# Optimization experiments

Measured on AMD Instinct MI355X. Metric: run time of the kernel, lower is better.

The kernel has to match this reference:

```python
import jax, jax.numpy as jnp
import numpy as np

N_NODES = 50000
N_EDGES = 800000
NUM_FEATURES = 128
DIM = 32
HEADS = 16
NUM_CLASSES = 2
NUM_GRAPHS = 64


def setup_inputs() -> dict:
    key = jax.random.key(0)
    ks = jax.random.split(key, 16)
    inv = lambda fan_in: 1.0 / np.sqrt(fan_in)
    inp = {
        "x": jax.random.normal(ks[0], (N_NODES, NUM_FEATURES), dtype=jnp.float32),
        "edge_index": jax.random.randint(ks[1], (2, N_EDGES), 0, N_NODES, dtype=jnp.int64),
        "batch": jnp.sort(jax.random.randint(ks[2], (N_NODES,), 0, NUM_GRAPHS, dtype=jnp.int64)),
        # conv1: GraphConv(num_features -> dim)
        "W1_rel": jax.random.uniform(ks[3], (NUM_FEATURES, DIM), jnp.float32, -inv(NUM_FEATURES), inv(NUM_FEATURES)),
        "b1_rel": jnp.zeros((DIM,), jnp.float32),
        "W1_root": jax.random.uniform(ks[4], (NUM_FEATURES, DIM), jnp.float32, -inv(NUM_FEATURES), inv(NUM_FEATURES)),
        # conv3: GATConv(dim -> dim, heads=16, concat)
        "Wg": jax.random.uniform(ks[5], (DIM, HEADS * DIM), jnp.float32, -inv(DIM), inv(DIM)),
        "att_src": jax.random.uniform(ks[6], (HEADS, DIM), jnp.float32, -inv(DIM), inv(DIM)),
        "att_dst": jax.random.uniform(ks[7], (HEADS, DIM), jnp.float32, -inv(DIM), inv(DIM)),
        "bg": jnp.zeros((HEADS * DIM,), jnp.float32),
        # conv5: GraphConv(dim*16 -> dim)
        "W5_rel": jax.random.uniform(ks[8], (HEADS * DIM, DIM), jnp.float32, -inv(HEADS * DIM), inv(HEADS * DIM)),
        "b5_rel": jnp.zeros((DIM,), jnp.float32),
        "W5_root": jax.random.uniform(ks[9], (HEADS * DIM, DIM), jnp.float32, -inv(HEADS * DIM), inv(HEADS * DIM)),
        # fc1, fc2
        "Wfc1": jax.random.uniform(ks[10], (DIM, DIM), jnp.float32, -inv(DIM), inv(DIM)),
        "bfc1": jnp.zeros((DIM,), jnp.float32),
        "Wfc2": jax.random.uniform(ks[11], (DIM, NUM_CLASSES), jnp.float32, -inv(DIM), inv(DIM)),
        "bfc2": jnp.zeros((NUM_CLASSES,), jnp.float32),
    }
    return inp


def _graph_conv(x, src, dst, W_rel, b_rel, W_root):
    # PyG GraphConv (aggr='add'): out = lin_rel(sum_{j->i} x_j) + lin_root(x_i)
    agg = jax.ops.segment_sum(x[src], dst, num_segments=N_NODES)
    return agg @ W_rel + b_rel + x @ W_root


def _gat_conv(x, src, dst, W, att_src, att_dst, b):
    # PyG GATConv with add_self_loops=True, concat=True, negative_slope=0.2.
    # Dropout on attention is inactive in eval mode.
    loops = jnp.arange(N_NODES, dtype=src.dtype)
    src = jnp.concatenate([src, loops])
    dst = jnp.concatenate([dst, loops])
    h = (x @ W).reshape(N_NODES, HEADS, DIM)            # [N,H,C]
    a_src = jnp.einsum("nhc,hc->nh", h, att_src)        # [N,H]
    a_dst = jnp.einsum("nhc,hc->nh", h, att_dst)
    e = jax.nn.leaky_relu(a_src[src] + a_dst[dst], 0.2)  # [E,H]
    # segment softmax over incoming edges of each destination node
    e_max = jax.ops.segment_max(e, dst, num_segments=N_NODES)
    e_max = jnp.where(jnp.isfinite(e_max), e_max, 0.0)
    ex = jnp.exp(e - e_max[dst])
    denom = jax.ops.segment_sum(ex, dst, num_segments=N_NODES)
    alpha = ex / (denom[dst] + 1e-16)                   # [E,H]
    out = jax.ops.segment_sum(alpha[:, :, None] * h[src], dst, num_segments=N_NODES)
    return out.reshape(N_NODES, HEADS * DIM) + b


def reference(x, edge_index, batch, W1_rel, b1_rel, W1_root, Wg, att_src, att_dst, bg,
              W5_rel, b5_rel, W5_root, Wfc1, bfc1, Wfc2, bfc2):
    src, dst = edge_index[0], edge_index[1]
    h = jax.nn.relu(_graph_conv(x, src, dst, W1_rel, b1_rel, W1_root))
    h = jax.nn.relu(_gat_conv(h, src, dst, Wg, att_src, att_dst, bg))
    h = jax.nn.relu(_graph_conv(h, src, dst, W5_rel, b5_rel, W5_root))
    g = jax.ops.segment_sum(h, batch, num_segments=NUM_GRAPHS)  # global_add_pool
    g = jax.nn.relu(g @ Wfc1 + bfc1)
    logits = g @ Wfc2 + bfc2
    return jax.nn.sigmoid(logits)
```

## Files before the change

kernel.cpp:

```cpp
#include <hip/hip_runtime.h>

#define N_NODES 50000
#define N_EDGES 800000
#define NFEAT 128
#define DIM 32
#define HEADS 16
#define NGRAPH 64


__device__ inline bool edges_are_i64(const int* raw) {
    int acc = 0;
#pragma unroll
    for (int i = 1; i < 16; i += 2) acc |= raw[2 * N_EDGES - 16 + i];
    return acc == 0;
}

__global__ __launch_bounds__(256) void decode_edges(const int* __restrict__ raw,
                                                    int* __restrict__ esrc,
                                                    int* __restrict__ edst) {
    const bool is64 = edges_are_i64(raw);
    int e = blockIdx.x * 256 + threadIdx.x;
    if (e < N_EDGES) {
        if (is64) { esrc[e] = raw[2 * e]; edst[e] = raw[2 * (N_EDGES + e)]; }
        else      { esrc[e] = raw[e];     edst[e] = raw[N_EDGES + e]; }
    }
}

__global__ __launch_bounds__(256) void decode_batch(const int* __restrict__ raw,
                                                    int* __restrict__ out) {
    int acc = 0;
#pragma unroll
    for (int i = 1; i < 16; i += 2) acc |= raw[N_NODES - 16 + i];
    const bool is64 = (acc == 0);
    int b = blockIdx.x * 256 + threadIdx.x;
    if (b < N_NODES) {
        int v = is64 ? raw[2 * b] : raw[b];
        out[b] = v < 0 ? 0 : (v >= NGRAPH ? NGRAPH - 1 : v);
    }
}

__global__ __launch_bounds__(256) void init_kernel(int* __restrict__ deg, float* __restrict__ gpool) {
    int i = blockIdx.x * 256 + threadIdx.x;
    if (i < N_NODES) deg[i] = 1;
    if (i < NGRAPH * DIM) gpool[i] = 0.f;
}

__device__ inline int clampN(int v) {
    return v < 0 ? 0 : (v >= N_NODES ? N_NODES - 1 : v);
}

__global__ __launch_bounds__(256) void hist_kernel(const int* __restrict__ edst, int* __restrict__ deg) {
    int e = blockIdx.x * 256 + threadIdx.x;
    if (e < N_EDGES) atomicAdd(&deg[clampN(edst[e])], 1);
}

__global__ __launch_bounds__(1024) void scan_kernel(const int* __restrict__ deg,
                                                    int* __restrict__ off, int* __restrict__ cur) {
    __shared__ int part[1024];
    const int t = threadIdx.x;
    const int CH = (N_NODES + 1023) / 1024;
    int b0 = t * CH, b1 = b0 + CH;
    if (b0 > N_NODES) b0 = N_NODES;
    if (b1 > N_NODES) b1 = N_NODES;
    int s = 0;
    for (int i = b0; i < b1; ++i) s += deg[i];
    part[t] = s;
    __syncthreads();
    for (int ofs = 1; ofs < 1024; ofs <<= 1) {
        int v = part[t];
        int u = (t >= ofs) ? part[t - ofs] : 0;
        __syncthreads();
        part[t] = v + u;
        __syncthreads();
    }
    int run = (t > 0) ? part[t - 1] : 0;
    for (int i = b0; i < b1; ++i) { off[i] = run; cur[i] = run; run += deg[i]; }
    if (t == 1023) off[N_NODES] = part[1023];
}

__global__ __launch_bounds__(256) void place_kernel(const int* __restrict__ esrc,
                                                    const int* __restrict__ edst,
                                                    int* __restrict__ cur, int* __restrict__ nbr) {
    int idx = blockIdx.x * 256 + threadIdx.x;
    if (idx >= N_EDGES + N_NODES) return;
    int d, v;
    if (idx < N_EDGES) { d = clampN(edst[idx]); v = clampN(esrc[idx]); }
    else { d = idx - N_EDGES; v = d; }
    int p = atomicAdd(&cur[d], 1);
    nbr[p] = v;
}

__global__ __launch_bounds__(256) void node_linear2(const float* __restrict__ x,
                                                    const float* __restrict__ Wa,
                                                    const float* __restrict__ Wb,
                                                    const float* __restrict__ bias_b,
                                                    float* __restrict__ xrb, int n) {
    constexpr int KC = 128;
    constexpr int NB = 8;
    __shared__ float sWt[2][32][KC + 4];
    __shared__ float sX[NB][KC];
    const int t = threadIdx.x;
    const int o = t & 63;
    const int mat = o >> 5;
    const int c = o & 31;
    const int sub = t >> 6;
    const int base = blockIdx.x * NB;

    for (int i = t; i < 2 * KC * 32; i += 256) {
        int m = i >= KC * 32;
        int j = i - m * KC * 32;
        int kk = j >> 5, cc = j & 31;
        sWt[m][cc][kk] = (m ? Wb : Wa)[kk * 32 + cc];
    }
    for (int i = t; i < NB * KC; i += 256) {
        int r = i >> 7, kk = i & (KC - 1);
        int node = base + r;
        sX[r][kk] = (node < n) ? x[(size_t)node * KC + kk] : 0.f;
    }
    __syncthreads();
    float acc[2] = {0.f, 0.f};
#pragma unroll 4
    for (int kv = 0; kv < KC / 4; ++kv) {
        const float4 w = *(const float4*)&sWt[mat][c][kv * 4];
#pragma unroll
        for (int s = 0; s < 2; ++s) {
            const float4 xv = *(const float4*)&sX[sub + s * 4][kv * 4];
            acc[s] += w.x * xv.x + w.y * xv.y + w.z * xv.z + w.w * xv.w;
        }
    }
    const float bb = (mat == 1) ? bias_b[c] : 0.f;
#pragma unroll
    for (int s = 0; s < 2; ++s) {
        int node = base + sub + s * 4;
        if (node < n) xrb[(size_t)node * 64 + mat * 32 + c] = acc[s] + bb;
    }
}

__global__ __launch_bounds__(256) void graphconv_gather(const float* __restrict__ xrb,
                                                        const int* __restrict__ off,
                                                        const int* __restrict__ nbr,
                                                        float* __restrict__ out) {
    int d = blockIdx.x * 4 + (threadIdx.x >> 6);
    if (d >= N_NODES) return;
    const int l = threadIdx.x & 63;
    const int c = l & 31, half = l >> 5;
    const int j0 = off[d], j1 = off[d + 1];
    float acc = 0.f;
    for (int j = j0 + half; j < j1; j += 2) acc += xrb[(size_t)nbr[j] * 64 + c];
    acc += __shfl_xor(acc, 32);
    acc += xrb[(size_t)d * 64 + 32 + c] - xrb[(size_t)d * 64 + c];
    if (half == 0) out[(size_t)d * 32 + c] = acc > 0.f ? acc : 0.f;
}

__global__ __launch_bounds__(1024) void attc_kernel(const float* __restrict__ Wg,
                                                    const float* __restrict__ attS,
                                                    const float* __restrict__ attD,
                                                    float* __restrict__ attc) {
    const int t = threadIdx.x;
    const int sd = t >> 9, k = (t >> 4) & 31, hd = t & 15;
    const float* att = sd ? attD : attS;
    float acc = 0.f;
#pragma unroll
    for (int c = 0; c < 32; ++c) acc += Wg[k * 512 + hd * 32 + c] * att[hd * 32 + c];
    attc[t] = acc;
}

__global__ __launch_bounds__(256) void gat_att(const float* __restrict__ h1,
                                               const float* __restrict__ attc,
                                               float* __restrict__ asrc,
                                               float* __restrict__ adst) {
    __shared__ float sh1[8][32];
    __shared__ float sattc[1024];
    const int t = threadIdx.x;
    for (int i = t; i < 1024; i += 256) sattc[i] = attc[i];
    {
        int n0 = t >> 5, k = t & 31;
        sh1[n0][k] = h1[(size_t)(blockIdx.x * 8 + n0) * 32 + k];
    }
    __syncthreads();
    const int nl = t >> 5, hd = (t >> 1) & 15, sd = t & 1;
    float acc = 0.f;
#pragma unroll
    for (int k = 0; k < 32; ++k) acc += sh1[nl][k] * sattc[sd * 512 + k * 16 + hd];
    (sd ? adst : asrc)[(size_t)(blockIdx.x * 8 + nl) * 16 + hd] = acc;
}

__global__ __launch_bounds__(512) void gat_mega(const float* __restrict__ h1,
                                                const float* __restrict__ asrc,
                                                const float* __restrict__ adst,
                                                const int* __restrict__ off,
                                                const int* __restrict__ nbr,
                                                const float* __restrict__ Wg,
                                                const float* __restrict__ bg,
                                                const float* __restrict__ W5_rel,
                                                const float* __restrict__ W5_root,
                                                const float* __restrict__ b5,
                                                float* __restrict__ xrb) {
    __shared__ float sh_agg[8][512];
    __shared__ float sh_h2[8][512];
    __shared__ float spart[8][8][64];
    const int t = threadIdx.x;
    const int w = t >> 6, l = t & 63;
    const int d = blockIdx.x * 8 + w;

    {
        const int hd = l & 15;
        const int kb = (l >> 4) << 3;
        const float adst_v = adst[(size_t)d * 16 + hd];
        const int j0 = off[d], j1 = off[d + 1];
        float m = -1e30f;
        for (int j = j0; j < j1; ++j) {
            int s = nbr[j];
            float e = asrc[(size_t)s * 16 + hd] + adst_v;
            e = e < 0.f ? 0.2f * e : e;
            m = fmaxf(m, e);
        }
        float den = 0.f;
        float4 acca = {0.f, 0.f, 0.f, 0.f}, accb = {0.f, 0.f, 0.f, 0.f};
        for (int j = j0; j < j1; ++j) {
            int s = nbr[j];
            float e = asrc[(size_t)s * 16 + hd] + adst_v;
            e = e < 0.f ? 0.2f * e : e;
            float ex = expf(e - m);
            den += ex;
            const float4 ha = *(const float4*)&h1[(size_t)s * 32 + kb];
            const float4 hb = *(const float4*)&h1[(size_t)s * 32 + kb + 4];
            acca.x += ex * ha.x; acca.y += ex * ha.y; acca.z += ex * ha.z; acca.w += ex * ha.w;
            accb.x += ex * hb.x; accb.y += ex * hb.y; accb.z += ex * hb.z; accb.w += ex * hb.w;
        }
        const float r = 1.f / (den + 1e-16f);
        acca.x *= r; acca.y *= r; acca.z *= r; acca.w *= r;
        accb.x *= r; accb.y *= r; accb.z *= r; accb.w *= r;
        *(float4*)&sh_agg[w][hd * 32 + kb] = acca;
        *(float4*)&sh_agg[w][hd * 32 + kb + 4] = accb;
    }
    __syncthreads();

    {
        const int hh = (t >> 5) << 5;
        float acc[8] = {0.f, 0.f, 0.f, 0.f, 0.f, 0.f, 0.f, 0.f};
        for (int k = 0; k < 32; ++k) {
            const float wv = Wg[k * 512 + t];
#pragma unroll
            for (int nl = 0; nl < 8; ++nl) acc[nl] += sh_agg[nl][hh + k] * wv;
        }
        const float bgv = bg[t];
#pragma unroll
        for (int nl = 0; nl < 8; ++nl) {
            float v = acc[nl] + bgv;
            sh_h2[nl][t] = v > 0.f ? v : 0.f;
        }
    }
    __syncthreads();

    {
        const float* wp = (l < 32) ? (W5_rel + l) : (W5_root + (l - 32));
        float acc[8] = {0.f, 0.f, 0.f, 0.f, 0.f, 0.f, 0.f, 0.f};
        const int c0 = w * 64;
        for (int cc = 0; cc < 64; ++cc) {
            const int col = c0 + cc;
            const float wv = wp[(size_t)col * 32];
#pragma unroll
            for (int nl = 0; nl < 8; ++nl) acc[nl] += sh_h2[nl][col] * wv;
        }
#pragma unroll
        for (int nl = 0; nl < 8; ++nl) spart[w][nl][l] = acc[nl];
    }
    __syncthreads();

    {
        float acc = (l >= 32) ? b5[l - 32] : 0.f;
#pragma unroll
        for (int ww = 0; ww < 8; ++ww) acc += spart[ww][w][l];
        xrb[(size_t)(blockIdx.x * 8 + w) * 64 + l] = acc;
    }
}

__global__ __launch_bounds__(256) void pool_kernel(const float* __restrict__ h3,
                                                   const int* __restrict__ batch,
                                                   float* __restrict__ g) {
    const int KRUN = 32;
    int c = threadIdx.x & 31;
    int grp = blockIdx.x * 8 + (threadIdx.x >> 5);
    int n0 = grp * KRUN;
    if (n0 >= N_NODES) return;
    int nend = n0 + KRUN;
    if (nend > N_NODES) nend = N_NODES;
    float acc = 0.f;
    int curb = -1;
    for (int nn = n0; nn < nend; ++nn) {
        int b = batch[nn];
        if (b != curb) {
            if (curb >= 0) atomicAdd(&g[curb * 32 + c], acc);
            acc = 0.f;
            curb = b;
        }
        acc += h3[(size_t)nn * 32 + c];
    }
    if (curb >= 0) atomicAdd(&g[curb * 32 + c], acc);
}

__global__ __launch_bounds__(256) void final_head(const float* __restrict__ g,
                                                  const float* __restrict__ Wfc1,
                                                  const float* __restrict__ bfc1,
                                                  const float* __restrict__ Wfc2,
                                                  const float* __restrict__ bfc2,
                                                  float* __restrict__ out) {
    __shared__ float sg[NGRAPH * 32];
    __shared__ float s1[NGRAPH * 32];
    const int t = threadIdx.x;
    for (int i = t; i < NGRAPH * 32; i += 256) sg[i] = g[i];
    __syncthreads();
    for (int i = t; i < NGRAPH * 32; i += 256) {
        int gi = i >> 5, c = i & 31;
        float acc = bfc1[c];
#pragma unroll
        for (int k = 0; k < 32; ++k) acc += sg[gi * 32 + k] * Wfc1[k * 32 + c];
        s1[i] = acc > 0.f ? acc : 0.f;
    }
    __syncthreads();
    if (t < NGRAPH * 2) {
        int gi = t >> 1, cls = t & 1;
        float acc = bfc2[cls];
#pragma unroll
        for (int k = 0; k < 32; ++k) acc += s1[gi * 32 + k] * Wfc2[k * 2 + cls];
        out[t] = 1.f / (1.f + expf(-acc));
    }
}

extern "C" void kernel_launch(void* const* d_in, const int* in_sizes, int n_in,
                              void* d_out, int out_size, void* d_ws, size_t ws_size,
                              hipStream_t stream) {
    const float* x       = (const float*)d_in[0];
    const int*   eraw    = (const int*)d_in[1];
    const int*   braw    = (const int*)d_in[2];
    const float* W1_rel  = (const float*)d_in[3];
    const float* b1_rel  = (const float*)d_in[4];
    const float* W1_root = (const float*)d_in[5];
    const float* Wg      = (const float*)d_in[6];
    const float* attS    = (const float*)d_in[7];
    const float* attD    = (const float*)d_in[8];
    const float* bg      = (const float*)d_in[9];
    const float* W5_rel  = (const float*)d_in[10];
    const float* b5_rel  = (const float*)d_in[11];
    const float* W5_root = (const float*)d_in[12];
    const float* Wfc1    = (const float*)d_in[13];
    const float* bfc1    = (const float*)d_in[14];
    const float* Wfc2    = (const float*)d_in[15];
    const float* bfc2    = (const float*)d_in[16];
    float* out = (float*)d_out;

    float* f     = (float*)d_ws;
    float* xrb   = f;
    float* h1    = xrb + (size_t)N_NODES * 64;
    float* asrc  = h1 + (size_t)N_NODES * 32;
    float* adst  = asrc + (size_t)N_NODES * 16;
    float* attc  = adst + (size_t)N_NODES * 16;
    float* gpool = attc + 1024;
    int* esrcd   = (int*)(gpool + 2048);
    int* edstd   = esrcd + N_EDGES;
    int* batchd  = edstd + N_EDGES;
    int* deg     = batchd + N_NODES;
    int* off     = deg + (N_NODES + 1);
    int* cur     = off + (N_NODES + 1);
    int* nbr     = cur + N_NODES;

    decode_edges<<<(N_EDGES + 255) / 256, 256, 0, stream>>>(eraw, esrcd, edstd);
    decode_batch<<<(N_NODES + 255) / 256, 256, 0, stream>>>(braw, batchd);
    init_kernel<<<(N_NODES + 255) / 256, 256, 0, stream>>>(deg, gpool);
    hist_kernel<<<(N_EDGES + 255) / 256, 256, 0, stream>>>(edstd, deg);
    scan_kernel<<<1, 1024, 0, stream>>>(deg, off, cur);
    place_kernel<<<(N_EDGES + N_NODES + 255) / 256, 256, 0, stream>>>(esrcd, edstd, cur, nbr);

    node_linear2<<<(N_NODES + 7) / 8, 256, 0, stream>>>(x, W1_rel, W1_root, b1_rel, xrb, N_NODES);
    graphconv_gather<<<(N_NODES + 3) / 4, 256, 0, stream>>>(xrb, off, nbr, h1);

    attc_kernel<<<1, 1024, 0, stream>>>(Wg, attS, attD, attc);
    gat_att<<<(N_NODES + 7) / 8, 256, 0, stream>>>(h1, attc, asrc, adst);
    gat_mega<<<N_NODES / 8, 512, 0, stream>>>(h1, asrc, adst, off, nbr, Wg, bg,
                                              W5_rel, W5_root, b5_rel, xrb);

    graphconv_gather<<<(N_NODES + 3) / 4, 256, 0, stream>>>(xrb, off, nbr, h1);

    pool_kernel<<<((N_NODES + 31) / 32 + 7) / 8, 256, 0, stream>>>(h1, batchd, gpool);
    final_head<<<1, 256, 0, stream>>>(gpool, Wfc1, bfc1, Wfc2, bfc2, out);
}
```

Before: 820.5 us.

## Split GAT megakernel into gather and FFN kernels, fuse histogram into decode

Splits the fused GAT kernel into a smaller-block attention gather that writes the per-node aggregate to a global buffer and a separate FFN kernel that applies Wg and the W5 projections. This is meant to raise occupancy for the latency-bound gather at the cost of an extra 100MB-scale round trip through memory. The split only runs when the workspace is large enough; otherwise the old megakernel, now with unrolled loops and reused shared memory, is used. The change also fuses the degree histogram into edge decoding, removes redundant clamps, and unrolls the graphconv gather loop to expose more memory-level parallelism.

```diff
diff --git a/kernel.cpp b/kernel.cpp
--- a/kernel.cpp
+++ b/kernel.cpp
@@ -1,4 +1,5 @@
 #include <hip/hip_runtime.h>
+#include <stdint.h>
 
 #define N_NODES 50000
 #define N_EDGES 800000
@@ -7,6 +8,11 @@
 #define HEADS 16
 #define NGRAPH 64
 
+__device__ inline int clampN(int v) {
+    return v < 0 ? 0 : (v >= N_NODES ? N_NODES - 1 : v);
+}
+
+__device__ inline float lrelu(float e) { return e < 0.f ? 0.2f * e : e; }
 
 __device__ inline bool edges_are_i64(const int* raw) {
     int acc = 0;
@@ -15,14 +21,19 @@
     return acc == 0;
 }
 
-__global__ __launch_bounds__(256) void decode_edges(const int* __restrict__ raw,
-                                                    int* __restrict__ esrc,
-                                                    int* __restrict__ edst) {
+__global__ __launch_bounds__(256) void decode_edges_hist(const int* __restrict__ raw,
+                                                         int* __restrict__ esrc,
+                                                         int* __restrict__ edst,
+                                                         int* __restrict__ deg) {
     const bool is64 = edges_are_i64(raw);
     int e = blockIdx.x * 256 + threadIdx.x;
     if (e < N_EDGES) {
-        if (is64) { esrc[e] = raw[2 * e]; edst[e] = raw[2 * (N_EDGES + e)]; }
-        else      { esrc[e] = raw[e];     edst[e] = raw[N_EDGES + e]; }
+        int s, d;
+        if (is64) { s = raw[2 * e]; d = raw[2 * (N_EDGES + e)]; }
+        else      { s = raw[e];     d = raw[N_EDGES + e]; }
+        s = clampN(s); d = clampN(d);
+        esrc[e] = s; edst[e] = d;
+        atomicAdd(&deg[d], 1);
     }
 }
 
@@ -43,15 +54,6 @@
     int i = blockIdx.x * 256 + threadIdx.x;
     if (i < N_NODES) deg[i] = 1;
     if (i < NGRAPH * DIM) gpool[i] = 0.f;
-}
-
-__device__ inline int clampN(int v) {
-    return v < 0 ? 0 : (v >= N_NODES ? N_NODES - 1 : v);
-}
-
-__global__ __launch_bounds__(256) void hist_kernel(const int* __restrict__ edst, int* __restrict__ deg) {
-    int e = blockIdx.x * 256 + threadIdx.x;
-    if (e < N_EDGES) atomicAdd(&deg[clampN(edst[e])], 1);
 }
 
 __global__ __launch_bounds__(1024) void scan_kernel(const int* __restrict__ deg,
@@ -84,7 +86,7 @@
     int idx = blockIdx.x * 256 + threadIdx.x;
     if (idx >= N_EDGES + N_NODES) return;
     int d, v;
-    if (idx < N_EDGES) { d = clampN(edst[idx]); v = clampN(esrc[idx]); }
+    if (idx < N_EDGES) { d = edst[idx]; v = esrc[idx]; }
     else { d = idx - N_EDGES; v = d; }
     int p = atomicAdd(&cur[d], 1);
     nbr[p] = v;
@@ -146,7 +148,16 @@
     const int c = l & 31, half = l >> 5;
     const int j0 = off[d], j1 = off[d + 1];
     float acc = 0.f;
-    for (int j = j0 + half; j < j1; j += 2) acc += xrb[(size_t)nbr[j] * 64 + c];
+    int j = j0 + half;
+    for (; j + 6 < j1; j += 8) {
+        int s0 = nbr[j], s1 = nbr[j + 2], s2 = nbr[j + 4], s3 = nbr[j + 6];
+        float v0 = xrb[(size_t)s0 * 64 + c];
+        float v1 = xrb[(size_t)s1 * 64 + c];
+        float v2 = xrb[(size_t)s2 * 64 + c];
+        float v3 = xrb[(size_t)s3 * 64 + c];
+        acc += (v0 + v1) + (v2 + v3);
+    }
+    for (; j < j1; j += 2) acc += xrb[(size_t)nbr[j] * 64 + c];
     acc += __shfl_xor(acc, 32);
     acc += xrb[(size_t)d * 64 + 32 + c] - xrb[(size_t)d * 64 + c];
     if (half == 0) out[(size_t)d * 32 + c] = acc > 0.f ? acc : 0.f;
@@ -183,6 +194,131 @@
 #pragma unroll
     for (int k = 0; k < 32; ++k) acc += sh1[nl][k] * sattc[sd * 512 + k * 16 + hd];
     (sd ? adst : asrc)[(size_t)(blockIdx.x * 8 + nl) * 16 + hd] = acc;
+}
+
+__global__ __launch_bounds__(256) void gat_gather(const float* __restrict__ h1,
+                                                  const float* __restrict__ asrc,
+                                                  const float* __restrict__ adst,
+                                                  const int* __restrict__ off,
+                                                  const int* __restrict__ nbr,
+                                                  float* __restrict__ agg) {
+    const int d = blockIdx.x * 4 + (threadIdx.x >> 6);
+    const int l = threadIdx.x & 63;
+    const int hd = l >> 2;
+    const int kb = (l & 3) << 3;
+    const float adst_v = adst[(size_t)d * 16 + hd];
+    const int j0 = off[d], j1 = off[d + 1];
+
+    float m = -1e30f;
+    int j = j0;
+    for (; j + 4 <= j1; j += 4) {
+        int s0 = nbr[j], s1 = nbr[j + 1], s2 = nbr[j + 2], s3 = nbr[j + 3];
+        float e0 = lrelu(asrc[(size_t)s0 * 16 + hd] + adst_v);
+        float e1 = lrelu(asrc[(size_t)s1 * 16 + hd] + adst_v);
+        float e2 = lrelu(asrc[(size_t)s2 * 16 + hd] + adst_v);
+        float e3 = lrelu(asrc[(size_t)s3 * 16 + hd] + adst_v);
+        m = fmaxf(m, fmaxf(fmaxf(e0, e1), fmaxf(e2, e3)));
+    }
+    for (; j < j1; ++j)
+        m = fmaxf(m, lrelu(asrc[(size_t)nbr[j] * 16 + hd] + adst_v));
+
+    float den = 0.f;
+    float a0x = 0.f, a0y = 0.f, a0z = 0.f, a0w = 0.f;
+    float a1x = 0.f, a1y = 0.f, a1z = 0.f, a1w = 0.f;
+    j = j0;
+    for (; j + 2 <= j1; j += 2) {
+        int s0 = nbr[j], s1 = nbr[j + 1];
+        float e0 = lrelu(asrc[(size_t)s0 * 16 + hd] + adst_v);
+        float e1 = lrelu(asrc[(size_t)s1 * 16 + hd] + adst_v);
+        float ex0 = expf(e0 - m), ex1 = expf(e1 - m);
+        den += ex0 + ex1;
+        const float4 h00 = *(const float4*)&h1[(size_t)s0 * 32 + kb];
+        const float4 h01 = *(const float4*)&h1[(size_t)s0 * 32 + kb + 4];
+        const float4 h10 = *(const float4*)&h1[(size_t)s1 * 32 + kb];
+        const float4 h11 = *(const float4*)&h1[(size_t)s1 * 32 + kb + 4];
+        a0x += ex0 * h00.x + ex1 * h10.x; a0y += ex0 * h00.y + ex1 * h10.y;
+        a0z += ex0 * h00.z + ex1 * h10.z; a0w += ex0 * h00.w + ex1 * h10.w;
+        a1x += ex0 * h01.x + ex1 * h11.x; a1y += ex0 * h01.y + ex1 * h11.y;
+        a1z += ex0 * h01.z + ex1 * h11.z; a1w += ex0 * h01.w + ex1 * h11.w;
+    }
+    if (j < j1) {
+        int s0 = nbr[j];
+        float e0 = lrelu(asrc[(size_t)s0 * 16 + hd] + adst_v);
+        float ex0 = expf(e0 - m);
+        den += ex0;
+        const float4 h00 = *(const float4*)&h1[(size_t)s0 * 32 + kb];
+        const float4 h01 = *(const float4*)&h1[(size_t)s0 * 32 + kb + 4];
+        a0x += ex0 * h00.x; a0y += ex0 * h00.y; a0z += ex0 * h00.z; a0w += ex0 * h00.w;
+        a1x += ex0 * h01.x; a1y += ex0 * h01.y; a1z += ex0 * h01.z; a1w += ex0 * h01.w;
+    }
+    const float r = 1.f / (den + 1e-16f);
+    float* ap = agg + (size_t)d * 512 + 8 * l;
+    float4 o0 = {a0x * r, a0y * r, a0z * r, a0w * r};
+    float4 o1 = {a1x * r, a1y * r, a1z * r, a1w * r};
+    *(float4*)ap = o0;
+    *(float4*)(ap + 4) = o1;
+}
+
+__global__ __launch_bounds__(512) void gat_ffn(const float* __restrict__ agg,
+                                               const float* __restrict__ Wg,
+                                               const float* __restrict__ bg,
+                                               const float* __restrict__ W5_rel,
+                                               const float* __restrict__ W5_root,
+                                               const float* __restrict__ b5,
+                                               float* __restrict__ xrb) {
+    __shared__ float sA[8][512];
+    __shared__ float sH[8][512];
+    const int t = threadIdx.x;
+    const int base = blockIdx.x * 8;
+
+    {
+        const float4* av = (const float4*)(agg + (size_t)base * 512);
+        float4* sv = (float4*)&sA[0][0];
+        sv[t] = av[t];
+        sv[t + 512] = av[t + 512];
+    }
+    __syncthreads();
+
+    {
+        const int hh = (t >> 5) << 5;
+        float acc[8] = {0.f, 0.f, 0.f, 0.f, 0.f, 0.f, 0.f, 0.f};
+        for (int k = 0; k < 32; ++k) {
+            const float wv = Wg[k * 512 + t];
+#pragma unroll
+            for (int nl = 0; nl < 8; ++nl) acc[nl] += sA[nl][hh + k] * wv;
+        }
+        const float bgv = bg[t];
+#pragma unroll
+        for (int nl = 0; nl < 8; ++nl) {
+            float v = acc[nl] + bgv;
+            sH[nl][t] = v > 0.f ? v : 0.f;
+        }
+    }
+    __syncthreads();
+
+    float* spart = &sA[0][0];
+    const int w = t >> 6, l = t & 63;
+    {
+        const float* wp = (l < 32) ? (W5_rel + l) : (W5_root + (l - 32));
+        float p[8] = {0.f, 0.f, 0.f, 0.f, 0.f, 0.f, 0.f, 0.f};
+        const int c0 = w * 64;
+        for (int cc = 0; cc < 64; ++cc) {
+            const int col = c0 + cc;
+            const float wv = wp[(size_t)col * 32];
+#pragma unroll
+            for (int nl = 0; nl < 8; ++nl) p[nl] += sH[nl][col] * wv;
+        }
+#pragma unroll
+        for (int nl = 0; nl < 8; ++nl) spart[(size_t)(w * 8 + nl) * 64 + l] = p[nl];
+    }
+    __syncthreads();
+
+    {
+        float acc = (l >= 32) ? b5[l - 32] : 0.f;
+#pragma unroll
+        for (int ww = 0; ww < 8; ++ww) acc += spart[(size_t)(ww * 8 + w) * 64 + l];
+        xrb[(size_t)(base + w) * 64 + l] = acc;
+    }
 }
 
 __global__ __launch_bounds__(512) void gat_mega(const float* __restrict__ h1,
@@ -198,41 +334,61 @@
                                                 float* __restrict__ xrb) {
     __shared__ float sh_agg[8][512];
     __shared__ float sh_h2[8][512];
-    __shared__ float spart[8][8][64];
     const int t = threadIdx.x;
     const int w = t >> 6, l = t & 63;
     const int d = blockIdx.x * 8 + w;
 
     {
-        const int hd = l & 15;
-        const int kb = (l >> 4) << 3;
+        const int hd = l >> 2;
+        const int kb = (l & 3) << 3;
         const float adst_v = adst[(size_t)d * 16 + hd];
         const int j0 = off[d], j1 = off[d + 1];
         float m = -1e30f;
-        for (int j = j0; j < j1; ++j) {
-            int s = nbr[j];
-            float e = asrc[(size_t)s * 16 + hd] + adst_v;
-            e = e < 0.f ? 0.2f * e : e;
-            m = fmaxf(m, e);
-        }
+        int j = j0;
+        for (; j + 4 <= j1; j += 4) {
+            int s0 = nbr[j], s1 = nbr[j + 1], s2 = nbr[j + 2], s3 = nbr[j + 3];
+            float e0 = lrelu(asrc[(size_t)s0 * 16 + hd] + adst_v);
+            float e1 = lrelu(asrc[(size_t)s1 * 16 + hd] + adst_v);
+            float e2 = lrelu(asrc[(size_t)s2 * 16 + hd] + adst_v);
+            float e3 = lrelu(asrc[(size_t)s3 * 16 + hd] + adst_v);
+            m = fmaxf(m, fmaxf(fmaxf(e0, e1), fmaxf(e2, e3)));
+        }
+        for (; j < j1; ++j)
+            m = fmaxf(m, lrelu(asrc[(size_t)nbr[j] * 16 + hd] + adst_v));
+
         float den = 0.f;
-        float4 acca = {0.f, 0.f, 0.f, 0.f}, accb = {0.f, 0.f, 0.f, 0.f};
-        for (int j = j0; j < j1; ++j) {
-            int s = nbr[j];
-            float e = asrc[(size_t)s * 16 + hd] + adst_v;
-            e = e < 0.f ? 0.2f * e : e;
-            float ex = expf(e - m);
-            den += ex;
-            const float4 ha = *(const float4*)&h1[(size_t)s * 32 + kb];
-            const float4 hb = *(const float4*)&h1[(size_t)s * 32 + kb + 4];
-            acca.x += ex * ha.x; acca.y += ex * ha.y; acca.z += ex * ha.z; acca.w += ex * ha.w;
-            accb.x += ex * hb.x; accb.y += ex * hb.y; accb.z += ex * hb.z; accb.w += ex * hb.w;
+        float a0x = 0.f, a0y = 0.f, a0z = 0.f, a0w = 0.f;
+        float a1x = 0.f, a1y = 0.f, a1z = 0.f, a1w = 0.f;
+        j = j0;
+        for (; j + 2 <= j1; j += 2) {
+            int s0 = nbr[j], s1 = nbr[j + 1];
+            float e0 = lrelu(asrc[(size_t)s0 * 16 + hd] + adst_v);
+            float e1 = lrelu(asrc[(size_t)s1 * 16 + hd] + adst_v);
+            float ex0 = expf(e0 - m), ex1 = expf(e1 - m);
+            den += ex0 + ex1;
+            const float4 h00 = *(const float4*)&h1[(size_t)s0 * 32 + kb];
+            const float4 h01 = *(const float4*)&h1[(size_t)s0 * 32 + kb + 4];
+            const float4 h10 = *(const float4*)&h1[(size_t)s1 * 32 + kb];
+            const float4 h11 = *(const float4*)&h1[(size_t)s1 * 32 + kb + 4];
+            a0x += ex0 * h00.x + ex1 * h10.x; a0y += ex0 * h00.y + ex1 * h10.y;
+            a0z += ex0 * h00.z + ex1 * h10.z; a0w += ex0 * h00.w + ex1 * h10.w;
+            a1x += ex0 * h01.x + ex1 * h11.x; a1y += ex0 * h01.y + ex1 * h11.y;
+            a1z += ex0 * h01.z + ex1 * h11.z; a1w += ex0 * h01.w + ex1 * h11.w;
+        }
+        if (j < j1) {
+            int s0 = nbr[j];
+            float e0 = lrelu(asrc[(size_t)s0 * 16 + hd] + adst_v);
+            float ex0 = expf(e0 - m);
+            den += ex0;
+            const float4 h00 = *(const float4*)&h1[(size_t)s0 * 32 + kb];
+            const float4 h01 = *(const float4*)&h1[(size_t)s0 * 32 + kb + 4];
+            a0x += ex0 * h00.x; a0y += ex0 * h00.y; a0z += ex0 * h00.z; a0w += ex0 * h00.w;
+            a1x += ex0 * h01.x; a1y += ex0 * h01.y; a1z += ex0 * h01.z; a1w += ex0 * h01.w;
         }
         const float r = 1.f / (den + 1e-16f);
-        acca.x *= r; acca.y *= r; acca.z *= r; acca.w *= r;
-        accb.x *= r; accb.y *= r; accb.z *= r; accb.w *= r;
-        *(float4*)&sh_agg[w][hd * 32 + kb] = acca;
-        *(float4*)&sh_agg[w][hd * 32 + kb + 4] = accb;
+        float* ap = &sh_agg[w][8 * l];
+        ap[0] = a0x * r; ap[1] = a0y * r; ap[2] = a0z * r; ap[3] = a0w * r;
+        ap[4] = a1x * r; ap[5] = a1y * r; ap[6] = a1z * r; ap[7] = a1w * r;
     }
     __syncthreads();
 
@@ -253,25 +409,26 @@
     }
     __syncthreads();
 
+    float* spart = &sh_agg[0][0];
     {
         const float* wp = (l < 32) ? (W5_rel + l) : (W5_root + (l - 32));
-        float acc[8] = {0.f, 0.f, 0.f, 0.f, 0.f, 0.f, 0.f, 0.f};
+        float p[8] = {0.f, 0.f, 0.f, 0.f, 0.f, 0.f, 0.f, 0.f};
         const int c0 = w * 64;
         for (int cc = 0; cc < 64; ++cc) {
             const int col = c0 + cc;
             const float wv = wp[(size_t)col * 32];
 #pragma unroll
-            for (int nl = 0; nl < 8; ++nl) acc[nl] += sh_h2[nl][col] * wv;
-        }
-#pragma unroll
-        for (int nl = 0; nl < 8; ++nl) spart[w][nl][l] = acc[nl];
+            for (int nl = 0; nl < 8; ++nl) p[nl] += sh_h2[nl][col] * wv;
+        }
+#pragma unroll
+        for (int nl = 0; nl < 8; ++nl) spart[(size_t)(w * 8 + nl) * 64 + l] = p[nl];
     }
     __syncthreads();
 
     {
         float acc = (l >= 32) ? b5[l - 32] : 0.f;
 #pragma unroll
-        for (int ww = 0; ww < 8; ++ww) acc += spart[ww][w][l];
+        for (int ww = 0; ww < 8; ++ww) acc += spart[(size_t)(ww * 8 + w) * 64 + l];
         xrb[(size_t)(blockIdx.x * 8 + w) * 64 + l] = acc;
     }
 }
@@ -364,11 +521,15 @@
     int* off     = deg + (N_NODES + 1);
     int* cur     = off + (N_NODES + 1);
     int* nbr     = cur + N_NODES;
-
-    decode_edges<<<(N_EDGES + 255) / 256, 256, 0, stream>>>(eraw, esrcd, edstd);
+    uintptr_t aggp = (uintptr_t)(nbr + (N_EDGES + N_NODES));
+    aggp = (aggp + 15) & ~(uintptr_t)15;
+    float* agg = (float*)aggp;
+    const size_t need_split = (aggp - (uintptr_t)d_ws) + (size_t)N_NODES * 512 * 4;
+    const bool use_split = ws_size >= need_split;
+
+    init_kernel<<<(N_NODES + 255) / 256, 256, 0, stream>>>(deg, gpool);
+    decode_edges_hist<<<(N_EDGES + 255) / 256, 256, 0, stream>>>(eraw, esrcd, edstd, deg);
     decode_batch<<<(N_NODES + 255) / 256, 256, 0, stream>>>(braw, batchd);
-    init_kernel<<<(N_NODES + 255) / 256, 256, 0, stream>>>(deg, gpool);
-    hist_kernel<<<(N_EDGES + 255) / 256, 256, 0, stream>>>(edstd, deg);
     scan_kernel<<<1, 1024, 0, stream>>>(deg, off, cur);
     place_kernel<<<(N_EDGES + N_NODES + 255) / 256, 256, 0, stream>>>(esrcd, edstd, cur, nbr);
 
@@ -377,8 +538,13 @@
 
     attc_kernel<<<1, 1024, 0, stream>>>(Wg, attS, attD, attc);
     gat_att<<<(N_NODES + 7) / 8, 256, 0, stream>>>(h1, attc, asrc, adst);
-    gat_mega<<<N_NODES / 8, 512, 0, stream>>>(h1, asrc, adst, off, nbr, Wg, bg,
-                                              W5_rel, W5_root, b5_rel, xrb);
+    if (use_split) {
+        gat_gather<<<(N_NODES + 3) / 4, 256, 0, stream>>>(h1, asrc, adst, off, nbr, agg);
+        gat_ffn<<<N_NODES / 8, 512, 0, stream>>>(agg, Wg, bg, W5_rel, W5_root, b5_rel, xrb);
+    } else {
+        gat_mega<<<N_NODES / 8, 512, 0, stream>>>(h1, asrc, adst, off, nbr, Wg, bg,
+                                                  W5_rel, W5_root, b5_rel, xrb);
+    }
 
     graphconv_gather<<<(N_NODES + 3) / 4, 256, 0, stream>>>(xrb, off, nbr, h1);
 
```

New measurement: 696.4 us. 1.18x faster.
